# Optimization experiments

Measured on AMD Instinct MI355X. Metric: run time of the kernel, lower is better.

The kernel has to match this reference:

```python
import jax, jax.numpy as jnp
import numpy as np

B, D, H, W = 2, 16, 16, 16
N = D * H * W
CDESC = 64
TEMP = 0.07
TOPK = 24
RADIUS = 0.45


def flatten_spatial(x):
    # (B, C, D, H, W) -> (B, N, C)
    b, c = x.shape[:2]
    return x.reshape(b, c, -1).transpose(0, 2, 1)


def voxel_grid():
    # normalized voxel-center grid in [-1, 1], shape (3, D, H, W)
    zs = jnp.linspace(-1.0, 1.0, D)
    ys = jnp.linspace(-1.0, 1.0, H)
    xs = jnp.linspace(-1.0, 1.0, W)
    return jnp.stack(jnp.meshgrid(zs, ys, xs, indexing='ij'), axis=0)


def setup_inputs() -> dict:
    key = jax.random.key(0)
    ks = jax.random.split(key, 8)
    return {
        'src_canonical': jax.random.normal(ks[0], (B, 3, D, H, W), jnp.float32),
        'tgt_canonical': jax.random.normal(ks[1], (B, 3, D, H, W), jnp.float32),
        'src_desc': jax.random.normal(ks[2], (B, CDESC, D, H, W), jnp.float32),
        'tgt_desc': jax.random.normal(ks[3], (B, CDESC, D, H, W), jnp.float32),
        'src_mlogits': jax.random.normal(ks[4], (B, 2, D, H, W), jnp.float32),
        'tgt_mlogits': jax.random.normal(ks[5], (B, 2, D, H, W), jnp.float32),
        'src_unc': jax.random.uniform(ks[6], (B, 1, D, H, W), jnp.float32),
        'tgt_unc': jax.random.uniform(ks[7], (B, 1, D, H, W), jnp.float32),
    }


def reference(src_canonical, tgt_canonical, src_desc, tgt_desc,
              src_mlogits, tgt_mlogits, src_unc, tgt_unc):
    sc = flatten_spatial(src_canonical)  # (B, N, 3)
    tc = flatten_spatial(tgt_canonical)  # (B, N, 3)
    sd = flatten_spatial(src_desc)       # (B, N, C)
    td = flatten_spatial(tgt_desc)       # (B, N, C)

    # torch.cdist: Euclidean distance matrix (B, N, N)
    d2 = (jnp.sum(sc * sc, -1)[:, :, None]
          + jnp.sum(tc * tc, -1)[:, None, :]
          - 2.0 * jnp.einsum('bid,bjd->bij', sc, tc))
    dist = jnp.sqrt(jnp.maximum(d2, 1e-12))

    sim = jnp.einsum('bid,bjd->bij', sd, td)  # (B, N, N)

    k = min(TOPK, N)
    _, nn_idx = jax.lax.top_k(-dist, k)  # k smallest distances per row
    bidx = jnp.arange(B)[:, None, None]
    ridx = jnp.arange(N)[None, :, None]
    allowed = jnp.zeros((B, N, N), bool).at[bidx, ridx, nn_idx].set(True)
    allowed = allowed | (dist <= RADIUS)

    tgt_match = jax.nn.softmax(flatten_spatial(tgt_mlogits), axis=-1)[..., 0]  # (B, N)
    src_match = jax.nn.softmax(flatten_spatial(src_mlogits), axis=-1)[..., 0]  # (B, N)

    # (B, N, 1) + (B, 1, N) rank-1 uncertainty penalty
    unc = flatten_spatial(src_unc) + flatten_spatial(tgt_unc).transpose(0, 2, 1)

    scores = sim - dist - 0.1 * unc
    scores = jnp.where(allowed, scores, -10000.0)
    # legacy matchability score mode
    scores = scores + jnp.maximum(jnp.log(tgt_match), -20.0)[:, None, :]
    probs = jax.nn.softmax(scores / TEMP, axis=-1)
    probs = jnp.nan_to_num(probs, nan=0.0, posinf=0.0, neginf=0.0)

    tpos = voxel_grid().reshape(3, -1).T  # (N, 3)
    expected = jnp.einsum('bij,jd->bid', probs, tpos)  # (B, N, 3)
    src_pos = jnp.broadcast_to(tpos, (B, N, 3))

    disp = (expected - src_pos).transpose(0, 2, 1).reshape(B, 3, D, H, W)
    disp = jnp.nan_to_num(disp, nan=0.0, posinf=0.0, neginf=0.0)

    conf = (jnp.max(probs, axis=-1) * src_match).reshape(B, 1, D, H, W)

    ent = -jnp.sum(probs * jnp.log(jnp.clip(probs, 1e-12, None)), axis=-1)
    ent = jnp.nan_to_num(ent, nan=0.0, posinf=0.0, neginf=0.0).reshape(B, 1, D, H, W)

    return expected, disp, probs, conf, ent, src_pos
```

## Files before the change

### kernel.cpp

```cpp
#include <hip/hip_runtime.h>
#include <math.h>
#include <stddef.h>

#define NN    4096
#define BATCH 2
#define CD    64
#define KSEL  24
#define RAD2  0.2025f
#define NBINS 256
#define KBASE 1888
#define CCAP  128
#define LCAP  256

__device__ __forceinline__ int d2key(float d2) {
  int k = (int)(__float_as_uint(d2) >> 19) - KBASE;
  return k < 0 ? 0 : (k > NBINS - 1 ? NBINS - 1 : k);
}

__global__ __launch_bounds__(256)
void prep_all(const float* __restrict__ td, const float* __restrict__ sd,
              const float* __restrict__ tml, const float* __restrict__ tu,
              float* __restrict__ tdT, float* __restrict__ sdT,
              float* __restrict__ addj) {
  __shared__ float tile[64][65];
  int blk = blockIdx.x;
  if (blk < 256) {
    const float* src = (blk < 128) ? td  : sd;
    float*       dst = (blk < 128) ? tdT : sdT;
    int lb = blk & 127;
    int b  = lb >> 6;
    int j0 = (lb & 63) << 6;
    int jl = threadIdx.x & 63;
    int cq = threadIdx.x >> 6;
    const float* srcp = src + (size_t)b * CD * NN;
#pragma unroll
    for (int r = 0; r < 16; ++r) {
      int c = r * 4 + cq;
      tile[c][jl] = srcp[(size_t)c * NN + j0 + jl];
    }
    __syncthreads();
    float* dstp = dst + (size_t)b * NN * CD;
#pragma unroll
    for (int r = 0; r < 16; ++r) {
      int j = r * 4 + cq;
      dstp[(size_t)(j0 + j) * CD + jl] = tile[jl][j];
    }
  } else {
    int idx = (blk - 256) * 256 + threadIdx.x;
    if (idx < BATCH * NN) {
      int b = idx >> 12, j = idx & (NN - 1);
      float l0 = tml[(size_t)b * 2 * NN + j];
      float l1 = tml[(size_t)b * 2 * NN + NN + j];
      float x  = l1 - l0;
      float sp = fmaxf(x, 0.0f) + log1pf(expf(-fabsf(x)));
      addj[idx] = fmaxf(-sp, -20.0f) - 0.1f * tu[idx];
    }
  }
}

__global__ __launch_bounds__(256, 6)
void matcher_main(const float* __restrict__ sc, const float* __restrict__ tc,
                  const float* __restrict__ sd, const float* __restrict__ td,
                  const float* __restrict__ tdT, const float* __restrict__ sdT,
                  const float* __restrict__ addj,
                  const float* __restrict__ tml, const float* __restrict__ tu,
                  const float* __restrict__ sml,
                  float* __restrict__ oexp, float* __restrict__ odisp,
                  float* __restrict__ oprob, float* __restrict__ oconf,
                  float* __restrict__ oent, float* __restrict__ osrc) {
  __shared__ __align__(16) int   hist[4][NBINS];
  __shared__ __align__(16) float sdp[4][CD];
  __shared__ float cand_d[4][CCAP];
  __shared__ int   cand_j[4][CCAP];
  __shared__ int   jlist[4][LCAP];
  __shared__ float vlist[4][LCAP];
  __shared__ int   candn[4], lcount[4];
  __shared__ float sD24[4];

  const int tid  = threadIdx.x;
  const int w    = tid >> 6;
  const int lane = tid & 63;
  const int row  = blockIdx.x * 4 + w;
  const int b    = row >> 12;
  const int i    = row & (NN - 1);

  ((int4*)hist[w])[lane] = make_int4(0, 0, 0, 0);
  if (lane == 0) { candn[w] = 0; lcount[w] = 0; }
  if (sdT) sdp[w][lane] = sdT[((size_t)b * NN + i) * CD + lane];
  else     sdp[w][lane] = sd[(size_t)b * CD * NN + (size_t)lane * NN + i];
  const float s0 = sc[(size_t)b * 3 * NN + i];
  const float s1 = sc[(size_t)b * 3 * NN + NN + i];
  const float s2 = sc[(size_t)b * 3 * NN + 2 * NN + i];
  __threadfence_block();

  const float4* tcx = (const float4*)(tc + (size_t)b * 3 * NN);
  const float4* tcy = tcx + NN / 4;
  const float4* tcz = tcy + NN / 4;
  float4* prow4 = (float4*)(oprob + (size_t)row * NN);
  float4 z4; z4.x = z4.y = z4.z = z4.w = 0.0f;

#pragma unroll 4
  for (int k = 0; k < 16; ++k) {
    int g = (k << 6) + lane;
    float4 X = tcx[g], Y = tcy[g], Z = tcz[g];
    prow4[g] = z4;
    float xs[4] = {X.x, X.y, X.z, X.w};
    float ys[4] = {Y.x, Y.y, Y.z, Y.w};
    float zs[4] = {Z.x, Z.y, Z.z, Z.w};
#pragma unroll
    for (int r = 0; r < 4; ++r) {
      float dx = xs[r] - s0, dy = ys[r] - s1, dz = zs[r] - s2;
      float d2 = fmaxf(__fmaf_rn(dx, dx, __fmaf_rn(dy, dy, dz * dz)), 1e-12f);
      atomicAdd(&hist[w][d2key(d2)], 1);
    }
  }
  __threadfence_block();

  int4 h4 = ((int4*)hist[w])[lane];
  int hv[4] = {h4.x, h4.y, h4.z, h4.w};
  int s = hv[0] + hv[1] + hv[2] + hv[3];
  int inc = s;
#pragma unroll
  for (int off = 1; off < 64; off <<= 1) {
    int t = __shfl_up(inc, off);
    if (lane >= off) inc += t;
  }
  int pre = inc - s;
  int Bl = -1, Bb = 0, below = pre;
#pragma unroll
  for (int q = 0; q < 4; ++q) {
    if (Bl < 0 && below < KSEL && below + hv[q] >= KSEL) { Bl = 4 * lane + q; Bb = below; }
    below += hv[q];
  }
  unsigned long long mk = __ballot(Bl >= 0);
  int srcl = __ffsll(mk) - 1;
  const int Bstar = __shfl(Bl, srcl);
  const int cb    = __shfl(Bb, srcl);
  const int Krem  = KSEL - cb;
  if (lane == 0) sD24[w] = __uint_as_float((unsigned)(Bstar + KBASE + 1) << 19);

#pragma unroll 4
  for (int k = 0; k < 16; ++k) {
    int g = (k << 6) + lane;
    float4 X = tcx[g], Y = tcy[g], Z = tcz[g];
    float xs[4] = {X.x, X.y, X.z, X.w};
    float ys[4] = {Y.x, Y.y, Y.z, Y.w};
    float zs[4] = {Z.x, Z.y, Z.z, Z.w};
#pragma unroll
    for (int r = 0; r < 4; ++r) {
      float dx = xs[r] - s0, dy = ys[r] - s1, dz = zs[r] - s2;
      float d2 = fmaxf(__fmaf_rn(dx, dx, __fmaf_rn(dy, dy, dz * dz)), 1e-12f);
      int key = d2key(d2);
      int j = (g << 2) + r;
      if (key == Bstar) {
        int c = atomicAdd(&candn[w], 1);
        if (c < CCAP) { cand_d[w][c] = d2; cand_j[w][c] = j; }
      } else if (key < Bstar || d2 <= RAD2) {
        int c = atomicAdd(&lcount[w], 1);
        if (c < LCAP) { jlist[w][c] = j; vlist[w][c] = d2; }
      }
    }
  }
  __threadfence_block();

  int nc = candn[w]; nc = nc > CCAP ? CCAP : nc;
  for (int e = lane; e < nc; e += 64) {
    float v = cand_d[w][e];
    int lt = 0, le = 0;
    for (int m = 0; m < nc; ++m) { float u = cand_d[w][m]; lt += (u < v); le += (u <= v); }
    if (lt < Krem && le >= Krem) sD24[w] = v;
  }
  __threadfence_block();
  const float thr2 = fmaxf(sD24[w], RAD2);
  for (int e = lane; e < nc; e += 64) {
    float v = cand_d[w][e];
    if (v <= thr2) {
      int c = atomicAdd(&lcount[w], 1);
      if (c < LCAP) { jlist[w][c] = cand_j[w][e]; vlist[w][c] = v; }
    }
  }
  __threadfence_block();
  int na = lcount[w]; na = na > LCAP ? LCAP : na;

  const float* tdb = tdT ? tdT + (size_t)b * NN * CD : nullptr;
  const float4* sdp4 = (const float4*)sdp[w];
  float mloc = -1e30f;
  for (int e = lane; e < na; e += 64) {
    int j = jlist[w][e];
    float d2 = vlist[w][e];
    float sim = 0.0f;
    if (tdb) {
      const float4* trow = (const float4*)(tdb + (size_t)j * CD);
#pragma unroll
      for (int q = 0; q < CD / 4; ++q) {
        float4 a = sdp4[q], t = trow[q];
        sim = fmaf(a.x, t.x, fmaf(a.y, t.y, fmaf(a.z, t.z, fmaf(a.w, t.w, sim))));
      }
    } else {
      const float* spx = (const float*)sdp4;
      const float* tp  = td + (size_t)b * CD * NN + j;
#pragma unroll 8
      for (int c = 0; c < CD; ++c) sim = fmaf(spx[c], tp[(size_t)c * NN], sim);
    }
    float aj;
    if (addj) {
      aj = addj[(size_t)b * NN + j];
    } else {
      float l0 = tml[(size_t)b * 2 * NN + j];
      float l1 = tml[(size_t)b * 2 * NN + NN + j];
      float x  = l1 - l0;
      float sp = fmaxf(x, 0.0f) + log1pf(expf(-fabsf(x)));
      aj = fmaxf(-sp, -20.0f) - 0.1f * tu[(size_t)b * NN + j];
    }
    float sco = sim - sqrtf(d2) + aj;
    vlist[w][e] = sco;
    mloc = fmaxf(mloc, sco);
  }
#pragma unroll
  for (int off = 32; off; off >>= 1) mloc = fmaxf(mloc, __shfl_xor(mloc, off));
  const float m = mloc;

  const float C1 = (1.0f / 0.07f) * 1.44269504089f;
  float zl = 0.0f, evu = 0.0f, evm = 0.0f;
  for (int e = lane; e < na; e += 64) {
    float u  = (vlist[w][e] - m) * C1;
    float ev = exp2f(u);
    vlist[w][e] = ev;
    zl  += ev;
    evu  = fmaf(ev, u, evu);
    evm  = fmaxf(evm, ev);
  }
#pragma unroll
  for (int off = 32; off; off >>= 1) {
    zl  += __shfl_xor(zl, off);
    evu += __shfl_xor(evu, off);
    evm  = fmaxf(evm, __shfl_xor(evm, off));
  }
  const float Z = zl, invZ = 1.0f / zl;

  __builtin_amdgcn_s_waitcnt(0x0F70);

  const float STEP = 2.0f / 15.0f;
  float ex0 = 0.f, ex1 = 0.f, ex2 = 0.f;
  for (int e = lane; e < na; e += 64) {
    float p = vlist[w][e] * invZ;
    int j = jlist[w][e];
    oprob[(size_t)row * NN + j] = p;
    float pz = -1.0f + STEP * (float)(j >> 8);
    float py = -1.0f + STEP * (float)((j >> 4) & 15);
    float px = -1.0f + STEP * (float)(j & 15);
    ex0 = fmaf(p, pz, ex0); ex1 = fmaf(p, py, ex1); ex2 = fmaf(p, px, ex2);
  }
#pragma unroll
  for (int off = 32; off; off >>= 1) {
    ex0 += __shfl_xor(ex0, off);
    ex1 += __shfl_xor(ex1, off);
    ex2 += __shfl_xor(ex2, off);
  }

  if (lane == 0) {
    const float LN2 = 0.69314718056f;
    float ent = LN2 * (log2f(Z) - evu * invZ);
    float tz = -1.0f + STEP * (float)(i >> 8);
    float ty = -1.0f + STEP * (float)((i >> 4) & 15);
    float tx = -1.0f + STEP * (float)(i & 15);
    size_t r3 = (size_t)row * 3;
    oexp[r3 + 0] = ex0; oexp[r3 + 1] = ex1; oexp[r3 + 2] = ex2;
    osrc[r3 + 0] = tz;  osrc[r3 + 1] = ty;  osrc[r3 + 2] = tx;
    size_t db = (size_t)b * 3 * NN;
    odisp[db + 0 * NN + i] = ex0 - tz;
    odisp[db + 1 * NN + i] = ex1 - ty;
    odisp[db + 2 * NN + i] = ex2 - tx;
    float ls0 = sml[(size_t)b * 2 * NN + i];
    float ls1 = sml[(size_t)b * 2 * NN + NN + i];
    float smv = 1.0f / (1.0f + expf(ls1 - ls0));
    oconf[(size_t)b * NN + i] = (evm * invZ) * smv;
    oent[(size_t)b * NN + i]  = ent;
  }
}

extern "C" void kernel_launch(void* const* d_in, const int* in_sizes, int n_in,
                              void* d_out, int out_size, void* d_ws, size_t ws_size,
                              hipStream_t stream) {
  const float* sc  = (const float*)d_in[0];
  const float* tc  = (const float*)d_in[1];
  const float* sd  = (const float*)d_in[2];
  const float* td  = (const float*)d_in[3];
  const float* sml = (const float*)d_in[4];
  const float* tml = (const float*)d_in[5];
  const float* tu  = (const float*)d_in[7];

  float* out   = (float*)d_out;
  float* oexp  = out;
  float* odisp = oexp  + (size_t)BATCH * NN * 3;
  float* oprob = odisp + (size_t)BATCH * NN * 3;
  float* oconf = oprob + (size_t)BATCH * NN * NN;
  float* oent  = oconf + (size_t)BATCH * NN;
  float* osrc  = oent  + (size_t)BATCH * NN;

  size_t need = ((size_t)2 * BATCH * NN * CD + (size_t)BATCH * NN) * sizeof(float);
  float* tdT = nullptr;
  float* sdT = nullptr;
  float* adj = nullptr;
  if (ws_size >= need) {
    tdT = (float*)d_ws;
    sdT = tdT + (size_t)BATCH * NN * CD;
    adj = sdT + (size_t)BATCH * NN * CD;
    prep_all<<<256 + 32, 256, 0, stream>>>(td, sd, tml, tu, tdT, sdT, adj);
  }
  matcher_main<<<BATCH * NN / 4, 256, 0, stream>>>(sc, tc, sd, td, tdT, sdT, adj,
                                                   tml, tu, sml,
                                                   oexp, odisp, oprob, oconf, oent, osrc);
}
```

Baseline: 206.9 us.

## Persistent blocks with LDS-cached target coords and register-resident binary-search top-k threshold

The matcher becomes a persistent kernel of 512 blocks. Each block loads one batch's target coordinates into shared memory once, and each wave pulls rows from a global atomic work counter. Each lane now keeps its 64 squared distances in registers. The histogram with its shared-memory atomics and the candidate re-pass are replaced by a radius count followed by a bit-pattern binary search for the 24th-smallest threshold, and selected entries are compacted with ballot/popcount. This removes the repeated global reads of the coordinates and the shared atomics, but it raises register pressure (occupancy bound lowered to 2) and may run several full 64-element count passes per row.

```diff
diff --git a/kernel.cpp b/kernel.cpp
--- a/kernel.cpp
+++ b/kernel.cpp
@@ -7,21 +7,15 @@
 #define CD    64
 #define KSEL  24
 #define RAD2  0.2025f
-#define NBINS 256
-#define KBASE 1888
-#define CCAP  128
-#define LCAP  256
-
-__device__ __forceinline__ int d2key(float d2) {
-  int k = (int)(__float_as_uint(d2) >> 19) - KBASE;
-  return k < 0 ? 0 : (k > NBINS - 1 ? NBINS - 1 : k);
-}
+#define LCAP  224
+#define NBLK  512
+#define WPB   4
 
 __global__ __launch_bounds__(256)
 void prep_all(const float* __restrict__ td, const float* __restrict__ sd,
               const float* __restrict__ tml, const float* __restrict__ tu,
               float* __restrict__ tdT, float* __restrict__ sdT,
-              float* __restrict__ addj) {
+              float* __restrict__ addj, int* __restrict__ gcnt) {
   __shared__ float tile[64][65];
   int blk = blockIdx.x;
   if (blk < 256) {
@@ -55,227 +49,232 @@
       float sp = fmaxf(x, 0.0f) + log1pf(expf(-fabsf(x)));
       addj[idx] = fmaxf(-sp, -20.0f) - 0.1f * tu[idx];
     }
+    if (idx < BATCH) gcnt[idx] = 0;
   }
 }
 
-__global__ __launch_bounds__(256, 6)
+__global__ __launch_bounds__(256, 2)
 void matcher_main(const float* __restrict__ sc, const float* __restrict__ tc,
                   const float* __restrict__ sd, const float* __restrict__ td,
                   const float* __restrict__ tdT, const float* __restrict__ sdT,
                   const float* __restrict__ addj,
                   const float* __restrict__ tml, const float* __restrict__ tu,
-                  const float* __restrict__ sml,
+                  const float* __restrict__ sml, int* __restrict__ gcnt,
                   float* __restrict__ oexp, float* __restrict__ odisp,
                   float* __restrict__ oprob, float* __restrict__ oconf,
                   float* __restrict__ oent, float* __restrict__ osrc) {
-  __shared__ __align__(16) int   hist[4][NBINS];
-  __shared__ __align__(16) float sdp[4][CD];
-  __shared__ float cand_d[4][CCAP];
-  __shared__ int   cand_j[4][CCAP];
-  __shared__ int   jlist[4][LCAP];
-  __shared__ float vlist[4][LCAP];
-  __shared__ int   candn[4], lcount[4];
-  __shared__ float sD24[4];
+  __shared__ __align__(16) float ltc[3 * NN];
+  __shared__ __align__(16) float sdp[WPB][CD];
+  __shared__ __align__(16) int2  list[WPB][LCAP];
 
   const int tid  = threadIdx.x;
   const int w    = tid >> 6;
   const int lane = tid & 63;
-  const int row  = blockIdx.x * 4 + w;
-  const int b    = row >> 12;
-  const int i    = row & (NN - 1);
-
-  ((int4*)hist[w])[lane] = make_int4(0, 0, 0, 0);
-  if (lane == 0) { candn[w] = 0; lcount[w] = 0; }
-  if (sdT) sdp[w][lane] = sdT[((size_t)b * NN + i) * CD + lane];
-  else     sdp[w][lane] = sd[(size_t)b * CD * NN + (size_t)lane * NN + i];
-  const float s0 = sc[(size_t)b * 3 * NN + i];
-  const float s1 = sc[(size_t)b * 3 * NN + NN + i];
-  const float s2 = sc[(size_t)b * 3 * NN + 2 * NN + i];
-  __threadfence_block();
-
-  const float4* tcx = (const float4*)(tc + (size_t)b * 3 * NN);
-  const float4* tcy = tcx + NN / 4;
-  const float4* tcz = tcy + NN / 4;
-  float4* prow4 = (float4*)(oprob + (size_t)row * NN);
-  float4 z4; z4.x = z4.y = z4.z = z4.w = 0.0f;
-
-#pragma unroll 4
-  for (int k = 0; k < 16; ++k) {
-    int g = (k << 6) + lane;
-    float4 X = tcx[g], Y = tcy[g], Z = tcz[g];
-    prow4[g] = z4;
-    float xs[4] = {X.x, X.y, X.z, X.w};
-    float ys[4] = {Y.x, Y.y, Y.z, Y.w};
-    float zs[4] = {Z.x, Z.y, Z.z, Z.w};
-#pragma unroll
-    for (int r = 0; r < 4; ++r) {
-      float dx = xs[r] - s0, dy = ys[r] - s1, dz = zs[r] - s2;
-      float d2 = fmaxf(__fmaf_rn(dx, dx, __fmaf_rn(dy, dy, dz * dz)), 1e-12f);
-      atomicAdd(&hist[w][d2key(d2)], 1);
-    }
+  const int b    = blockIdx.x & 1;
+
+  {
+    const float4* g4 = (const float4*)(tc + (size_t)b * 3 * NN);
+    float4* l4 = (float4*)ltc;
+#pragma unroll
+    for (int q = 0; q < 12; ++q) l4[q * 256 + tid] = g4[q * 256 + tid];
   }
-  __threadfence_block();
-
-  int4 h4 = ((int4*)hist[w])[lane];
-  int hv[4] = {h4.x, h4.y, h4.z, h4.w};
-  int s = hv[0] + hv[1] + hv[2] + hv[3];
-  int inc = s;
-#pragma unroll
-  for (int off = 1; off < 64; off <<= 1) {
-    int t = __shfl_up(inc, off);
-    if (lane >= off) inc += t;
-  }
-  int pre = inc - s;
-  int Bl = -1, Bb = 0, below = pre;
-#pragma unroll
-  for (int q = 0; q < 4; ++q) {
-    if (Bl < 0 && below < KSEL && below + hv[q] >= KSEL) { Bl = 4 * lane + q; Bb = below; }
-    below += hv[q];
-  }
-  unsigned long long mk = __ballot(Bl >= 0);
-  int srcl = __ffsll(mk) - 1;
-  const int Bstar = __shfl(Bl, srcl);
-  const int cb    = __shfl(Bb, srcl);
-  const int Krem  = KSEL - cb;
-  if (lane == 0) sD24[w] = __uint_as_float((unsigned)(Bstar + KBASE + 1) << 19);
-
-#pragma unroll 4
-  for (int k = 0; k < 16; ++k) {
-    int g = (k << 6) + lane;
-    float4 X = tcx[g], Y = tcy[g], Z = tcz[g];
-    float xs[4] = {X.x, X.y, X.z, X.w};
-    float ys[4] = {Y.x, Y.y, Y.z, Y.w};
-    float zs[4] = {Z.x, Z.y, Z.z, Z.w};
-#pragma unroll
-    for (int r = 0; r < 4; ++r) {
-      float dx = xs[r] - s0, dy = ys[r] - s1, dz = zs[r] - s2;
-      float d2 = fmaxf(__fmaf_rn(dx, dx, __fmaf_rn(dy, dy, dz * dz)), 1e-12f);
-      int key = d2key(d2);
-      int j = (g << 2) + r;
-      if (key == Bstar) {
-        int c = atomicAdd(&candn[w], 1);
-        if (c < CCAP) { cand_d[w][c] = d2; cand_j[w][c] = j; }
-      } else if (key < Bstar || d2 <= RAD2) {
-        int c = atomicAdd(&lcount[w], 1);
-        if (c < LCAP) { jlist[w][c] = j; vlist[w][c] = d2; }
-      }
-    }
-  }
-  __threadfence_block();
-
-  int nc = candn[w]; nc = nc > CCAP ? CCAP : nc;
-  for (int e = lane; e < nc; e += 64) {
-    float v = cand_d[w][e];
-    int lt = 0, le = 0;
-    for (int m = 0; m < nc; ++m) { float u = cand_d[w][m]; lt += (u < v); le += (u <= v); }
-    if (lt < Krem && le >= Krem) sD24[w] = v;
-  }
-  __threadfence_block();
-  const float thr2 = fmaxf(sD24[w], RAD2);
-  for (int e = lane; e < nc; e += 64) {
-    float v = cand_d[w][e];
-    if (v <= thr2) {
-      int c = atomicAdd(&lcount[w], 1);
-      if (c < LCAP) { jlist[w][c] = cand_j[w][e]; vlist[w][c] = v; }
-    }
-  }
-  __threadfence_block();
-  int na = lcount[w]; na = na > LCAP ? LCAP : na;
-
+  __syncthreads();
+
+  const float4* lx = (const float4*)ltc;
+  const float4* ly = (const float4*)(ltc + NN);
+  const float4* lz = (const float4*)(ltc + 2 * NN);
   const float* tdb = tdT ? tdT + (size_t)b * NN * CD : nullptr;
-  const float4* sdp4 = (const float4*)sdp[w];
-  float mloc = -1e30f;
-  for (int e = lane; e < na; e += 64) {
-    int j = jlist[w][e];
-    float d2 = vlist[w][e];
-    float sim = 0.0f;
-    if (tdb) {
-      const float4* trow = (const float4*)(tdb + (size_t)j * CD);
-#pragma unroll
-      for (int q = 0; q < CD / 4; ++q) {
-        float4 a = sdp4[q], t = trow[q];
-        sim = fmaf(a.x, t.x, fmaf(a.y, t.y, fmaf(a.z, t.z, fmaf(a.w, t.w, sim))));
-      }
+  const float* scb = sc + (size_t)b * 3 * NN;
+
+  int it = 0;
+  for (;;) {
+    int row_l;
+    if (gcnt) {
+      if (lane == 0) row_l = atomicAdd(&gcnt[b], 1);
+      row_l = __shfl(row_l, 0);
     } else {
-      const float* spx = (const float*)sdp4;
-      const float* tp  = td + (size_t)b * CD * NN + j;
+      row_l = ((blockIdx.x >> 1) * WPB + w) + it * ((NBLK / 2) * WPB);
+      ++it;
+    }
+    if (row_l >= NN) break;
+    const int i   = row_l;
+    const int row = b * NN + i;
+
+    const float s0 = scb[i], s1 = scb[NN + i], s2 = scb[2 * NN + i];
+    sdp[w][lane] = sdT ? sdT[((size_t)b * NN + i) * CD + lane]
+                       : sd[(size_t)b * CD * NN + (size_t)lane * NN + i];
+
+    unsigned d2b[64];
+    int crad = 0;
+    float4* prow4 = (float4*)(oprob + (size_t)row * NN);
+    float4 z4; z4.x = z4.y = z4.z = z4.w = 0.0f;
+#pragma unroll
+    for (int k = 0; k < 16; ++k) {
+      int g = (k << 6) + lane;
+      float4 X = lx[g], Y = ly[g], Z = lz[g];
+      prow4[g] = z4;
+      float xs[4] = {X.x, X.y, X.z, X.w};
+      float ys[4] = {Y.x, Y.y, Y.z, Y.w};
+      float zs[4] = {Z.x, Z.y, Z.z, Z.w};
+#pragma unroll
+      for (int r = 0; r < 4; ++r) {
+        float dx = xs[r] - s0, dy = ys[r] - s1, dz = zs[r] - s2;
+        float d2 = fmaxf(__fmaf_rn(dx, dx, __fmaf_rn(dy, dy, dz * dz)), 1e-12f);
+        d2b[4 * k + r] = __float_as_uint(d2);
+        crad += (d2 <= RAD2);
+      }
+    }
+#pragma unroll
+    for (int off = 32; off; off >>= 1) crad += __shfl_xor(crad, off);
+
+    auto countle = [&](unsigned mb) -> int {
+      int c = 0;
+#pragma unroll
+      for (int m = 0; m < 64; ++m) c += (d2b[m] <= mb);
+#pragma unroll
+      for (int off = 32; off; off >>= 1) c += __shfl_xor(c, off);
+      return c;
+    };
+
+    unsigned thr;
+    if (crad >= KSEL) {
+      thr = __float_as_uint(RAD2);
+    } else {
+      unsigned lo = __float_as_uint(RAD2);
+      unsigned hi = 0x7f800000u;
+      int c = crad;
+      float t = RAD2;
+#pragma unroll 1
+      for (int p = 0; p < 6; ++p) {
+        t *= 4.0f;
+        unsigned tb = __float_as_uint(t);
+        c = countle(tb);
+        if (c >= KSEL) { hi = tb; break; }
+        lo = tb;
+      }
+      if (c == KSEL) {
+        thr = hi;
+      } else {
+#pragma unroll 1
+        while (lo + 1u < hi) {
+          unsigned mid = (lo + hi) >> 1;
+          int cm = countle(mid);
+          if (cm >= KSEL) { hi = mid; if (cm == KSEL) break; }
+          else lo = mid;
+        }
+        thr = hi;
+      }
+    }
+
+    int base = 0;
+#pragma unroll
+    for (int m = 0; m < 64; ++m) {
+      bool p = (d2b[m] <= thr);
+      unsigned long long mk = __ballot(p);
+      if (p) {
+        int idx = base + (int)__popcll(mk & ((1ull << lane) - 1ull));
+        int j = ((m >> 2) << 8) + (lane << 2) + (m & 3);
+        if (idx < LCAP) list[w][idx] = make_int2(j, (int)d2b[m]);
+      }
+      base += (int)__popcll(mk);
+    }
+    const int na = base < LCAP ? base : LCAP;
+
+    const float4* sp4 = (const float4*)sdp[w];
+    float mloc = -1e30f;
+    for (int e = lane; e < na; e += 64) {
+      int2 en = list[w][e];
+      int j = en.x;
+      float d2 = __uint_as_float((unsigned)en.y);
+      float sim = 0.0f;
+      if (tdb) {
+        const float4* trow = (const float4*)(tdb + (size_t)j * CD);
+#pragma unroll
+        for (int q = 0; q < CD / 4; ++q) {
+          float4 a = sp4[q], t4 = trow[q];
+          sim = fmaf(a.x, t4.x, fmaf(a.y, t4.y, fmaf(a.z, t4.z, fmaf(a.w, t4.w, sim))));
+        }
+      } else {
+        const float* spx = (const float*)sp4;
+        const float* tp  = td + (size_t)b * CD * NN + j;
 #pragma unroll 8
-      for (int c = 0; c < CD; ++c) sim = fmaf(spx[c], tp[(size_t)c * NN], sim);
-    }
-    float aj;
-    if (addj) {
-      aj = addj[(size_t)b * NN + j];
-    } else {
-      float l0 = tml[(size_t)b * 2 * NN + j];
-      float l1 = tml[(size_t)b * 2 * NN + NN + j];
-      float x  = l1 - l0;
-      float sp = fmaxf(x, 0.0f) + log1pf(expf(-fabsf(x)));
-      aj = fmaxf(-sp, -20.0f) - 0.1f * tu[(size_t)b * NN + j];
-    }
-    float sco = sim - sqrtf(d2) + aj;
-    vlist[w][e] = sco;
-    mloc = fmaxf(mloc, sco);
-  }
-#pragma unroll
-  for (int off = 32; off; off >>= 1) mloc = fmaxf(mloc, __shfl_xor(mloc, off));
-  const float m = mloc;
-
-  const float C1 = (1.0f / 0.07f) * 1.44269504089f;
-  float zl = 0.0f, evu = 0.0f, evm = 0.0f;
-  for (int e = lane; e < na; e += 64) {
-    float u  = (vlist[w][e] - m) * C1;
-    float ev = exp2f(u);
-    vlist[w][e] = ev;
-    zl  += ev;
-    evu  = fmaf(ev, u, evu);
-    evm  = fmaxf(evm, ev);
-  }
-#pragma unroll
-  for (int off = 32; off; off >>= 1) {
-    zl  += __shfl_xor(zl, off);
-    evu += __shfl_xor(evu, off);
-    evm  = fmaxf(evm, __shfl_xor(evm, off));
-  }
-  const float Z = zl, invZ = 1.0f / zl;
-
-  __builtin_amdgcn_s_waitcnt(0x0F70);
-
-  const float STEP = 2.0f / 15.0f;
-  float ex0 = 0.f, ex1 = 0.f, ex2 = 0.f;
-  for (int e = lane; e < na; e += 64) {
-    float p = vlist[w][e] * invZ;
-    int j = jlist[w][e];
-    oprob[(size_t)row * NN + j] = p;
-    float pz = -1.0f + STEP * (float)(j >> 8);
-    float py = -1.0f + STEP * (float)((j >> 4) & 15);
-    float px = -1.0f + STEP * (float)(j & 15);
-    ex0 = fmaf(p, pz, ex0); ex1 = fmaf(p, py, ex1); ex2 = fmaf(p, px, ex2);
-  }
-#pragma unroll
-  for (int off = 32; off; off >>= 1) {
-    ex0 += __shfl_xor(ex0, off);
-    ex1 += __shfl_xor(ex1, off);
-    ex2 += __shfl_xor(ex2, off);
-  }
-
-  if (lane == 0) {
-    const float LN2 = 0.69314718056f;
-    float ent = LN2 * (log2f(Z) - evu * invZ);
-    float tz = -1.0f + STEP * (float)(i >> 8);
-    float ty = -1.0f + STEP * (float)((i >> 4) & 15);
-    float tx = -1.0f + STEP * (float)(i & 15);
-    size_t r3 = (size_t)row * 3;
-    oexp[r3 + 0] = ex0; oexp[r3 + 1] = ex1; oexp[r3 + 2] = ex2;
-    osrc[r3 + 0] = tz;  osrc[r3 + 1] = ty;  osrc[r3 + 2] = tx;
-    size_t db = (size_t)b * 3 * NN;
-    odisp[db + 0 * NN + i] = ex0 - tz;
-    odisp[db + 1 * NN + i] = ex1 - ty;
-    odisp[db + 2 * NN + i] = ex2 - tx;
-    float ls0 = sml[(size_t)b * 2 * NN + i];
-    float ls1 = sml[(size_t)b * 2 * NN + NN + i];
-    float smv = 1.0f / (1.0f + expf(ls1 - ls0));
-    oconf[(size_t)b * NN + i] = (evm * invZ) * smv;
-    oent[(size_t)b * NN + i]  = ent;
+        for (int c2 = 0; c2 < CD; ++c2) sim = fmaf(spx[c2], tp[(size_t)c2 * NN], sim);
+      }
+      float aj;
+      if (addj) {
+        aj = addj[(size_t)b * NN + j];
+      } else {
+        float l0 = tml[(size_t)b * 2 * NN + j];
+        float l1 = tml[(size_t)b * 2 * NN + NN + j];
+        float x  = l1 - l0;
+        float sp = fmaxf(x, 0.0f) + log1pf(expf(-fabsf(x)));
+        aj = fmaxf(-sp, -20.0f) - 0.1f * tu[(size_t)b * NN + j];
+      }
+      float sco = sim - sqrtf(d2) + aj;
+      list[w][e].y = __float_as_int(sco);
+      mloc = fmaxf(mloc, sco);
+    }
+#pragma unroll
+    for (int off = 32; off; off >>= 1) mloc = fmaxf(mloc, __shfl_xor(mloc, off));
+    const float m = mloc;
+
+    const float C1 = (1.0f / 0.07f) * 1.44269504089f;
+    float zl = 0.0f, evu = 0.0f, evm = 0.0f;
+    for (int e = lane; e < na; e += 64) {
+      float u  = (__int_as_float(list[w][e].y) - m) * C1;
+      float ev = exp2f(u);
+      list[w][e].y = __float_as_int(ev);
+      zl  += ev;
+      evu  = fmaf(ev, u, evu);
+      evm  = fmaxf(evm, ev);
+    }
+#pragma unroll
+    for (int off = 32; off; off >>= 1) {
+      zl  += __shfl_xor(zl, off);
+      evu += __shfl_xor(evu, off);
+      evm  = fmaxf(evm, __shfl_xor(evm, off));
+    }
+    const float Z = zl, invZ = 1.0f / zl;
+
+    __builtin_amdgcn_s_waitcnt(0x0F70);
+
+    const float STEP = 2.0f / 15.0f;
+    float ex0 = 0.f, ex1 = 0.f, ex2 = 0.f;
+    for (int e = lane; e < na; e += 64) {
+      float p = __int_as_float(list[w][e].y) * invZ;
+      int j = list[w][e].x;
+      oprob[(size_t)row * NN + j] = p;
+      float pz = -1.0f + STEP * (float)(j >> 8);
+      float py = -1.0f + STEP * (float)((j >> 4) & 15);
+      float px = -1.0f + STEP * (float)(j & 15);
+      ex0 = fmaf(p, pz, ex0); ex1 = fmaf(p, py, ex1); ex2 = fmaf(p, px, ex2);
+    }
+#pragma unroll
+    for (int off = 32; off; off >>= 1) {
+      ex0 += __shfl_xor(ex0, off);
+      ex1 += __shfl_xor(ex1, off);
+      ex2 += __shfl_xor(ex2, off);
+    }
+
+    if (lane == 0) {
+      const float LN2 = 0.69314718056f;
+      float ent = LN2 * (log2f(Z) - evu * invZ);
+      float tz = -1.0f + STEP * (float)(i >> 8);
+      float ty = -1.0f + STEP * (float)((i >> 4) & 15);
+      float tx = -1.0f + STEP * (float)(i & 15);
+      size_t r3 = (size_t)row * 3;
+      oexp[r3 + 0] = ex0; oexp[r3 + 1] = ex1; oexp[r3 + 2] = ex2;
+      osrc[r3 + 0] = tz;  osrc[r3 + 1] = ty;  osrc[r3 + 2] = tx;
+      size_t db = (size_t)b * 3 * NN;
+      odisp[db + 0 * NN + i] = ex0 - tz;
+      odisp[db + 1 * NN + i] = ex1 - ty;
+      odisp[db + 2 * NN + i] = ex2 - tx;
+      float ls0 = sml[(size_t)b * 2 * NN + i];
+      float ls1 = sml[(size_t)b * 2 * NN + NN + i];
+      float smv = 1.0f / (1.0f + expf(ls1 - ls0));
+      oconf[(size_t)b * NN + i] = (evm * invZ) * smv;
+      oent[(size_t)b * NN + i]  = ent;
+    }
   }
 }
 
@@ -298,17 +297,16 @@
   float* oent  = oconf + (size_t)BATCH * NN;
   float* osrc  = oent  + (size_t)BATCH * NN;
 
-  size_t need = ((size_t)2 * BATCH * NN * CD + (size_t)BATCH * NN) * sizeof(float);
-  float* tdT = nullptr;
-  float* sdT = nullptr;
-  float* adj = nullptr;
+  size_t need = ((size_t)2 * BATCH * NN * CD + (size_t)BATCH * NN) * sizeof(float)
+              + BATCH * sizeof(int);
+  float* tdT = nullptr; float* sdT = nullptr; float* adj = nullptr; int* gcnt = nullptr;
   if (ws_size >= need) {
-    tdT = (float*)d_ws;
-    sdT = tdT + (size_t)BATCH * NN * CD;
-    adj = sdT + (size_t)BATCH * NN * CD;
-    prep_all<<<256 + 32, 256, 0, stream>>>(td, sd, tml, tu, tdT, sdT, adj);
+    tdT  = (float*)d_ws;
+    sdT  = tdT + (size_t)BATCH * NN * CD;
+    adj  = sdT + (size_t)BATCH * NN * CD;
+    gcnt = (int*)(adj + (size_t)BATCH * NN);
+    prep_all<<<256 + 32, 256, 0, stream>>>(td, sd, tml, tu, tdT, sdT, adj, gcnt);
   }
-  matcher_main<<<BATCH * NN / 4, 256, 0, stream>>>(sc, tc, sd, td, tdT, sdT, adj,
-                                                   tml, tu, sml,
-                                                   oexp, odisp, oprob, oconf, oent, osrc);
+  matcher_main<<<NBLK, 256, 0, stream>>>(sc, tc, sd, td, tdT, sdT, adj, tml, tu, sml, gcnt,
+                                         oexp, odisp, oprob, oconf, oent, osrc);
 }
```

Result: slower. 256.0 us (+23.7%).

## Process one row per block, cache distances, write prob row densely once

Applied to the files above, without the earlier changes.

Each row is now handled by a whole 256-thread block instead of one wavefront, which cuts the per-thread work on each row by four. Squared distances stay in registers between the histogram pass and the selection pass, so they are not recomputed. A per-row byte index map in shared memory lets every prob element be written exactly once, as a dense nontemporal vector store, replacing a zero-fill followed by scattered writes. Entropy and max-prob are now computed directly from the probabilities. The cost is more block-wide syncs, and the selected-candidate list is capped at 255 entries so its index fits in a byte.

```diff
diff --git a/kernel.cpp b/kernel.cpp
--- a/kernel.cpp
+++ b/kernel.cpp
@@ -10,10 +10,12 @@
 #define NBINS 256
 #define KBASE 1888
 #define CCAP  128
-#define LCAP  256
-
-__device__ __forceinline__ int d2key(float d2) {
-  int k = (int)(__float_as_uint(d2) >> 19) - KBASE;
+#define LCAP  255
+
+typedef float f4v __attribute__((ext_vector_type(4)));
+
+__device__ __forceinline__ int d2key(unsigned bits) {
+  int k = (int)(bits >> 19) - KBASE;
   return k < 0 ? 0 : (k > NBINS - 1 ? NBINS - 1 : k);
 }
 
@@ -58,7 +60,7 @@
   }
 }
 
-__global__ __launch_bounds__(256, 6)
+__global__ __launch_bounds__(256, 8)
 void matcher_main(const float* __restrict__ sc, const float* __restrict__ tc,
                   const float* __restrict__ sd, const float* __restrict__ td,
                   const float* __restrict__ tdT, const float* __restrict__ sdT,
@@ -68,80 +70,43 @@
                   float* __restrict__ oexp, float* __restrict__ odisp,
                   float* __restrict__ oprob, float* __restrict__ oconf,
                   float* __restrict__ oent, float* __restrict__ osrc) {
-  __shared__ __align__(16) int   hist[4][NBINS];
-  __shared__ __align__(16) float sdp[4][CD];
-  __shared__ float cand_d[4][CCAP];
-  __shared__ int   cand_j[4][CCAP];
-  __shared__ int   jlist[4][LCAP];
-  __shared__ float vlist[4][LCAP];
-  __shared__ int   candn[4], lcount[4];
-  __shared__ float sD24[4];
+  __shared__ __align__(16) unsigned idxb32[NN / 4];
+  __shared__ __align__(16) int      hist[NBINS];
+  __shared__ __align__(16) float4   sdp4[CD / 4];
+  __shared__ float    pv[LCAP + 1];
+  __shared__ int2     jl[LCAP];
+  __shared__ unsigned cand[CCAP];
+  __shared__ float    red[4][8];
+  __shared__ float    fbuf[4];
+  __shared__ int      wtot[4];
+  __shared__ int      candn, lcount, sBin, sBelow;
+  __shared__ float    sD24;
 
   const int tid  = threadIdx.x;
   const int w    = tid >> 6;
   const int lane = tid & 63;
-  const int row  = blockIdx.x * 4 + w;
+  const int row  = blockIdx.x;
   const int b    = row >> 12;
   const int i    = row & (NN - 1);
 
-  ((int4*)hist[w])[lane] = make_int4(0, 0, 0, 0);
-  if (lane == 0) { candn[w] = 0; lcount[w] = 0; }
-  if (sdT) sdp[w][lane] = sdT[((size_t)b * NN + i) * CD + lane];
-  else     sdp[w][lane] = sd[(size_t)b * CD * NN + (size_t)lane * NN + i];
-  const float s0 = sc[(size_t)b * 3 * NN + i];
-  const float s1 = sc[(size_t)b * 3 * NN + NN + i];
-  const float s2 = sc[(size_t)b * 3 * NN + 2 * NN + i];
-  __threadfence_block();
-
+  if (tid < 64) ((int4*)hist)[tid] = make_int4(0, 0, 0, 0);
+#pragma unroll
+  for (int q = 0; q < 4; ++q) idxb32[(q << 8) + tid] = 0u;
+  if (sdT) { if (tid < 16) sdp4[tid] = ((const float4*)(sdT + ((size_t)b * NN + i) * CD))[tid]; }
+  else     { if (tid < 64) ((float*)sdp4)[tid] = sd[(size_t)b * CD * NN + (size_t)tid * NN + i]; }
+  if (tid == 0) { candn = 0; lcount = 0; sBin = -1; sBelow = 0; }
+
+  const float* scb = sc + (size_t)b * 3 * NN;
+  const float s0 = scb[i], s1 = scb[NN + i], s2 = scb[2 * NN + i];
   const float4* tcx = (const float4*)(tc + (size_t)b * 3 * NN);
   const float4* tcy = tcx + NN / 4;
   const float4* tcz = tcy + NN / 4;
-  float4* prow4 = (float4*)(oprob + (size_t)row * NN);
-  float4 z4; z4.x = z4.y = z4.z = z4.w = 0.0f;
-
-#pragma unroll 4
-  for (int k = 0; k < 16; ++k) {
-    int g = (k << 6) + lane;
-    float4 X = tcx[g], Y = tcy[g], Z = tcz[g];
-    prow4[g] = z4;
-    float xs[4] = {X.x, X.y, X.z, X.w};
-    float ys[4] = {Y.x, Y.y, Y.z, Y.w};
-    float zs[4] = {Z.x, Z.y, Z.z, Z.w};
-#pragma unroll
-    for (int r = 0; r < 4; ++r) {
-      float dx = xs[r] - s0, dy = ys[r] - s1, dz = zs[r] - s2;
-      float d2 = fmaxf(__fmaf_rn(dx, dx, __fmaf_rn(dy, dy, dz * dz)), 1e-12f);
-      atomicAdd(&hist[w][d2key(d2)], 1);
-    }
-  }
-  __threadfence_block();
-
-  int4 h4 = ((int4*)hist[w])[lane];
-  int hv[4] = {h4.x, h4.y, h4.z, h4.w};
-  int s = hv[0] + hv[1] + hv[2] + hv[3];
-  int inc = s;
-#pragma unroll
-  for (int off = 1; off < 64; off <<= 1) {
-    int t = __shfl_up(inc, off);
-    if (lane >= off) inc += t;
-  }
-  int pre = inc - s;
-  int Bl = -1, Bb = 0, below = pre;
-#pragma unroll
-  for (int q = 0; q < 4; ++q) {
-    if (Bl < 0 && below < KSEL && below + hv[q] >= KSEL) { Bl = 4 * lane + q; Bb = below; }
-    below += hv[q];
-  }
-  unsigned long long mk = __ballot(Bl >= 0);
-  int srcl = __ffsll(mk) - 1;
-  const int Bstar = __shfl(Bl, srcl);
-  const int cb    = __shfl(Bb, srcl);
-  const int Krem  = KSEL - cb;
-  if (lane == 0) sD24[w] = __uint_as_float((unsigned)(Bstar + KBASE + 1) << 19);
-
-#pragma unroll 4
-  for (int k = 0; k < 16; ++k) {
-    int g = (k << 6) + lane;
+  __syncthreads();
+
+  unsigned d2b[16];
+#pragma unroll
+  for (int k = 0; k < 4; ++k) {
+    int g = (k << 8) + tid;
     float4 X = tcx[g], Y = tcy[g], Z = tcz[g];
     float xs[4] = {X.x, X.y, X.z, X.w};
     float ys[4] = {Y.x, Y.y, Y.z, Y.w};
@@ -150,132 +115,190 @@
     for (int r = 0; r < 4; ++r) {
       float dx = xs[r] - s0, dy = ys[r] - s1, dz = zs[r] - s2;
       float d2 = fmaxf(__fmaf_rn(dx, dx, __fmaf_rn(dy, dy, dz * dz)), 1e-12f);
-      int key = d2key(d2);
-      int j = (g << 2) + r;
-      if (key == Bstar) {
-        int c = atomicAdd(&candn[w], 1);
-        if (c < CCAP) { cand_d[w][c] = d2; cand_j[w][c] = j; }
-      } else if (key < Bstar || d2 <= RAD2) {
-        int c = atomicAdd(&lcount[w], 1);
-        if (c < LCAP) { jlist[w][c] = j; vlist[w][c] = d2; }
+      unsigned bits = __float_as_uint(d2);
+      d2b[(k << 2) + r] = bits;
+      atomicAdd(&hist[d2key(bits)], 1);
+    }
+  }
+  __syncthreads();
+
+  {
+    int h = hist[tid];
+    int inc = h;
+#pragma unroll
+    for (int off = 1; off < 64; off <<= 1) {
+      int t = __shfl_up(inc, off);
+      if (lane >= off) inc += t;
+    }
+    if (lane == 63) wtot[w] = inc;
+    __syncthreads();
+    int wb = 0;
+#pragma unroll
+    for (int ww = 0; ww < 4; ++ww) wb += (ww < w) ? wtot[ww] : 0;
+    int below = wb + inc - h;
+    if (below < KSEL && below + h >= KSEL) {
+      sBin = tid; sBelow = below;
+      sD24 = __uint_as_float((unsigned)(tid + KBASE + 1) << 19);
+    }
+    __syncthreads();
+  }
+  const int Bs = sBin, cb = sBelow;
+
+#pragma unroll
+  for (int m = 0; m < 16; ++m) {
+    if (d2key(d2b[m]) == Bs) {
+      int c = atomicAdd(&candn, 1);
+      if (c < CCAP) cand[c] = d2b[m];
+    }
+  }
+  __syncthreads();
+  {
+    int nc = candn < CCAP ? candn : CCAP;
+    int Krem = KSEL - cb;
+    if (tid < nc) {
+      unsigned v = cand[tid];
+      int lt = 0, le = 0;
+      for (int m = 0; m < nc; ++m) { unsigned u = cand[m]; lt += (u < v); le += (u <= v); }
+      if (lt < Krem && le >= Krem) sD24 = __uint_as_float(v);
+    }
+    __syncthreads();
+  }
+  const unsigned thrb = __float_as_uint(fmaxf(sD24, RAD2));
+
+#pragma unroll
+  for (int m = 0; m < 16; ++m) {
+    if (d2b[m] <= thrb) {
+      int idx = atomicAdd(&lcount, 1);
+      if (idx < LCAP) {
+        int j = ((m >> 2) << 10) + (tid << 2) + (m & 3);
+        ((unsigned char*)idxb32)[j] = (unsigned char)(idx + 1);
+        jl[idx] = make_int2(j, (int)d2b[m]);
       }
     }
   }
-  __threadfence_block();
-
-  int nc = candn[w]; nc = nc > CCAP ? CCAP : nc;
-  for (int e = lane; e < nc; e += 64) {
-    float v = cand_d[w][e];
-    int lt = 0, le = 0;
-    for (int m = 0; m < nc; ++m) { float u = cand_d[w][m]; lt += (u < v); le += (u <= v); }
-    if (lt < Krem && le >= Krem) sD24[w] = v;
-  }
-  __threadfence_block();
-  const float thr2 = fmaxf(sD24[w], RAD2);
-  for (int e = lane; e < nc; e += 64) {
-    float v = cand_d[w][e];
-    if (v <= thr2) {
-      int c = atomicAdd(&lcount[w], 1);
-      if (c < LCAP) { jlist[w][c] = cand_j[w][e]; vlist[w][c] = v; }
-    }
-  }
-  __threadfence_block();
-  int na = lcount[w]; na = na > LCAP ? LCAP : na;
+  __syncthreads();
+  const int na = lcount < LCAP ? lcount : LCAP;
 
   const float* tdb = tdT ? tdT + (size_t)b * NN * CD : nullptr;
-  const float4* sdp4 = (const float4*)sdp[w];
-  float mloc = -1e30f;
-  for (int e = lane; e < na; e += 64) {
-    int j = jlist[w][e];
-    float d2 = vlist[w][e];
-    float sim = 0.0f;
+  float sco = -1e30f;
+  int   jme = 0;
+  if (tid < na) {
+    int2 en = jl[tid];
+    jme = en.x;
+    float d2 = __uint_as_float((unsigned)en.y);
+    float a0 = 0.f, a1 = 0.f, a2 = 0.f, a3 = 0.f;
     if (tdb) {
-      const float4* trow = (const float4*)(tdb + (size_t)j * CD);
-#pragma unroll
-      for (int q = 0; q < CD / 4; ++q) {
-        float4 a = sdp4[q], t = trow[q];
-        sim = fmaf(a.x, t.x, fmaf(a.y, t.y, fmaf(a.z, t.z, fmaf(a.w, t.w, sim))));
+      const float4* trow = (const float4*)(tdb + (size_t)jme * CD);
+#pragma unroll
+      for (int q = 0; q < CD / 4; q += 4) {
+        float4 x0 = sdp4[q],     t0 = trow[q];
+        float4 x1 = sdp4[q + 1], t1 = trow[q + 1];
+        float4 x2 = sdp4[q + 2], t2 = trow[q + 2];
+        float4 x3 = sdp4[q + 3], t3 = trow[q + 3];
+        a0 = fmaf(x0.x, t0.x, fmaf(x0.y, t0.y, fmaf(x0.z, t0.z, fmaf(x0.w, t0.w, a0))));
+        a1 = fmaf(x1.x, t1.x, fmaf(x1.y, t1.y, fmaf(x1.z, t1.z, fmaf(x1.w, t1.w, a1))));
+        a2 = fmaf(x2.x, t2.x, fmaf(x2.y, t2.y, fmaf(x2.z, t2.z, fmaf(x2.w, t2.w, a2))));
+        a3 = fmaf(x3.x, t3.x, fmaf(x3.y, t3.y, fmaf(x3.z, t3.z, fmaf(x3.w, t3.w, a3))));
       }
     } else {
       const float* spx = (const float*)sdp4;
-      const float* tp  = td + (size_t)b * CD * NN + j;
+      const float* tp  = td + (size_t)b * CD * NN + jme;
 #pragma unroll 8
-      for (int c = 0; c < CD; ++c) sim = fmaf(spx[c], tp[(size_t)c * NN], sim);
-    }
+      for (int c2 = 0; c2 < CD; ++c2) a0 = fmaf(spx[c2], tp[(size_t)c2 * NN], a0);
+    }
+    float sim = (a0 + a1) + (a2 + a3);
     float aj;
     if (addj) {
-      aj = addj[(size_t)b * NN + j];
+      aj = addj[(size_t)b * NN + jme];
     } else {
-      float l0 = tml[(size_t)b * 2 * NN + j];
-      float l1 = tml[(size_t)b * 2 * NN + NN + j];
+      float l0 = tml[(size_t)b * 2 * NN + jme];
+      float l1 = tml[(size_t)b * 2 * NN + NN + jme];
       float x  = l1 - l0;
       float sp = fmaxf(x, 0.0f) + log1pf(expf(-fabsf(x)));
-      aj = fmaxf(-sp, -20.0f) - 0.1f * tu[(size_t)b * NN + j];
-    }
-    float sco = sim - sqrtf(d2) + aj;
-    vlist[w][e] = sco;
-    mloc = fmaxf(mloc, sco);
-  }
-#pragma unroll
-  for (int off = 32; off; off >>= 1) mloc = fmaxf(mloc, __shfl_xor(mloc, off));
-  const float m = mloc;
-
+      aj = fmaxf(-sp, -20.0f) - 0.1f * tu[(size_t)b * NN + jme];
+    }
+    sco = sim - sqrtf(d2) + aj;
+  }
+  float mv = sco;
+#pragma unroll
+  for (int off = 32; off; off >>= 1) mv = fmaxf(mv, __shfl_xor(mv, off));
+  if (lane == 0) fbuf[w] = mv;
+  __syncthreads();
+  mv = fmaxf(fmaxf(fbuf[0], fbuf[1]), fmaxf(fbuf[2], fbuf[3]));
+  __syncthreads();
   const float C1 = (1.0f / 0.07f) * 1.44269504089f;
-  float zl = 0.0f, evu = 0.0f, evm = 0.0f;
-  for (int e = lane; e < na; e += 64) {
-    float u  = (vlist[w][e] - m) * C1;
-    float ev = exp2f(u);
-    vlist[w][e] = ev;
-    zl  += ev;
-    evu  = fmaf(ev, u, evu);
-    evm  = fmaxf(evm, ev);
-  }
-#pragma unroll
-  for (int off = 32; off; off >>= 1) {
-    zl  += __shfl_xor(zl, off);
-    evu += __shfl_xor(evu, off);
-    evm  = fmaxf(evm, __shfl_xor(evm, off));
-  }
-  const float Z = zl, invZ = 1.0f / zl;
-
-  __builtin_amdgcn_s_waitcnt(0x0F70);
+  float ev = 0.0f;
+  if (tid < na) ev = exp2f((sco - mv) * C1);
+  float zs = ev;
+#pragma unroll
+  for (int off = 32; off; off >>= 1) zs += __shfl_xor(zs, off);
+  if (lane == 0) fbuf[w] = zs;
+  __syncthreads();
+  const float Z = fbuf[0] + fbuf[1] + fbuf[2] + fbuf[3];
+  const float invZ = 1.0f / Z;
+  if (tid < na) pv[tid] = ev * invZ;
+  __syncthreads();
 
   const float STEP = 2.0f / 15.0f;
-  float ex0 = 0.f, ex1 = 0.f, ex2 = 0.f;
-  for (int e = lane; e < na; e += 64) {
-    float p = vlist[w][e] * invZ;
-    int j = jlist[w][e];
-    oprob[(size_t)row * NN + j] = p;
-    float pz = -1.0f + STEP * (float)(j >> 8);
-    float py = -1.0f + STEP * (float)((j >> 4) & 15);
-    float px = -1.0f + STEP * (float)(j & 15);
-    ex0 = fmaf(p, pz, ex0); ex1 = fmaf(p, py, ex1); ex2 = fmaf(p, px, ex2);
+  float ex0 = 0.f, ex1 = 0.f, ex2 = 0.f, pent = 0.f, pmax = 0.f;
+  f4v* prow4 = (f4v*)(oprob + (size_t)row * NN);
+#pragma unroll
+  for (int q = 0; q < 4; ++q) {
+    int c = (q << 8) + tid;
+    unsigned pk = idxb32[c];
+    f4v v;
+#pragma unroll
+    for (int r = 0; r < 4; ++r) {
+      unsigned u8 = (pk >> (8 * r)) & 0xFFu;
+      float p = 0.0f;
+      if (u8) {
+        p = pv[u8 - 1];
+        int j = (c << 2) + r;
+        float pz = -1.0f + STEP * (float)(j >> 8);
+        float py = -1.0f + STEP * (float)((j >> 4) & 15);
+        float px = -1.0f + STEP * (float)(j & 15);
+        ex0 = fmaf(p, pz, ex0); ex1 = fmaf(p, py, ex1); ex2 = fmaf(p, px, ex2);
+        pent = fmaf(p, logf(fmaxf(p, 1e-12f)), pent);
+        pmax = fmaxf(pmax, p);
+      }
+      v[r] = p;
+    }
+    __builtin_nontemporal_store(v, &prow4[c]);
   }
 #pragma unroll
   for (int off = 32; off; off >>= 1) {
     ex0 += __shfl_xor(ex0, off);
     ex1 += __shfl_xor(ex1, off);
     ex2 += __shfl_xor(ex2, off);
-  }
-
+    pent += __shfl_xor(pent, off);
+    pmax = fmaxf(pmax, __shfl_xor(pmax, off));
+  }
   if (lane == 0) {
-    const float LN2 = 0.69314718056f;
-    float ent = LN2 * (log2f(Z) - evu * invZ);
+    red[w][0] = ex0; red[w][1] = ex1; red[w][2] = ex2; red[w][3] = pent; red[w][4] = pmax;
+  }
+  __syncthreads();
+  if (tid == 0) {
+    float e0 = 0.f, e1 = 0.f, e2 = 0.f, pe = 0.f, pm = 0.f;
+#pragma unroll
+    for (int ww = 0; ww < 4; ++ww) {
+      e0 += red[ww][0]; e1 += red[ww][1]; e2 += red[ww][2]; pe += red[ww][3];
+      pm = fmaxf(pm, red[ww][4]);
+    }
     float tz = -1.0f + STEP * (float)(i >> 8);
     float ty = -1.0f + STEP * (float)((i >> 4) & 15);
     float tx = -1.0f + STEP * (float)(i & 15);
     size_t r3 = (size_t)row * 3;
-    oexp[r3 + 0] = ex0; oexp[r3 + 1] = ex1; oexp[r3 + 2] = ex2;
-    osrc[r3 + 0] = tz;  osrc[r3 + 1] = ty;  osrc[r3 + 2] = tx;
+    oexp[r3 + 0] = e0; oexp[r3 + 1] = e1; oexp[r3 + 2] = e2;
+    osrc[r3 + 0] = tz; osrc[r3 + 1] = ty; osrc[r3 + 2] = tx;
     size_t db = (size_t)b * 3 * NN;
-    odisp[db + 0 * NN + i] = ex0 - tz;
-    odisp[db + 1 * NN + i] = ex1 - ty;
-    odisp[db + 2 * NN + i] = ex2 - tx;
+    odisp[db + 0 * NN + i] = e0 - tz;
+    odisp[db + 1 * NN + i] = e1 - ty;
+    odisp[db + 2 * NN + i] = e2 - tx;
     float ls0 = sml[(size_t)b * 2 * NN + i];
     float ls1 = sml[(size_t)b * 2 * NN + NN + i];
     float smv = 1.0f / (1.0f + expf(ls1 - ls0));
-    oconf[(size_t)b * NN + i] = (evm * invZ) * smv;
-    oent[(size_t)b * NN + i]  = ent;
+    oconf[(size_t)b * NN + i] = pm * smv;
+    oent[(size_t)b * NN + i]  = -pe;
   }
 }
 
@@ -299,16 +322,14 @@
   float* osrc  = oent  + (size_t)BATCH * NN;
 
   size_t need = ((size_t)2 * BATCH * NN * CD + (size_t)BATCH * NN) * sizeof(float);
-  float* tdT = nullptr;
-  float* sdT = nullptr;
-  float* adj = nullptr;
+  float* tdT = nullptr; float* sdT = nullptr; float* adj = nullptr;
   if (ws_size >= need) {
     tdT = (float*)d_ws;
     sdT = tdT + (size_t)BATCH * NN * CD;
     adj = sdT + (size_t)BATCH * NN * CD;
     prep_all<<<256 + 32, 256, 0, stream>>>(td, sd, tml, tu, tdT, sdT, adj);
   }
-  matcher_main<<<BATCH * NN / 4, 256, 0, stream>>>(sc, tc, sd, td, tdT, sdT, adj,
-                                                   tml, tu, sml,
-                                                   oexp, odisp, oprob, oconf, oent, osrc);
+  matcher_main<<<BATCH * NN, 256, 0, stream>>>(sc, tc, sd, td, tdT, sdT, adj,
+                                               tml, tu, sml,
+                                               oexp, odisp, oprob, oconf, oent, osrc);
 }
```

New measurement: 201.7 us. 1.03x faster.
